# Performance work log

Hardware: AMD Instinct MI355X
Metric: run time of the kernel (lower is better)

## Reference

```python
import jax, jax.numpy as jnp
import numpy as np

N = 100000   # nodes
E = 600000   # edges
IN = 12      # in_dim
H = 128      # hidden_dim
OUT = 2      # out_dim
L = 3        # num_layers
EPS = 1e-5   # BatchNorm eps


def setup_inputs() -> dict:
    key = jax.random.key(0)
    ks = jax.random.split(key, 14)
    s = 0.05
    return {
        "features": jax.random.normal(ks[0], (N, IN), jnp.float32),
        "edge_index": jax.random.randint(ks[1], (2, E), 0, N, dtype=jnp.int32).astype(jnp.int64),
        "emb_W": jax.random.normal(ks[2], (IN, H), jnp.float32) * s,
        "emb_b": jnp.zeros((H,), jnp.float32),
        "Wself": jax.random.normal(ks[3], (L, H, H), jnp.float32) * s,
        "Wneigh": jax.random.normal(ks[4], (L, H, H), jnp.float32) * s,
        "conv_b": jnp.zeros((L, H), jnp.float32),
        "bn_gamma": jnp.ones((L, H), jnp.float32),
        "bn_beta": jnp.zeros((L, H), jnp.float32),
        "W1": jax.random.normal(ks[5], (H, H // 2), jnp.float32) * s,
        "b1": jnp.zeros((H // 2,), jnp.float32),
        "W2": jax.random.normal(ks[6], (H // 2, OUT), jnp.float32) * s,
        "b2": jnp.zeros((OUT,), jnp.float32),
    }


def reference(features, edge_index, emb_W, emb_b, Wself, Wneigh, conv_b,
              bn_gamma, bn_beta, W1, b1, W2, b2):
    src, dst = edge_index[0], edge_index[1]
    # in-degree per destination node (loop-invariant)
    deg = jax.ops.segment_sum(jnp.ones((E,), features.dtype), dst, num_segments=N)
    inv_deg = 1.0 / jnp.maximum(deg, 1.0)  # [N]

    h = features @ emb_W + emb_b           # embedding: [N, H]
    h_last = h
    for i in range(L):
        # SAGEConv 'mean': gather src feats, scatter-sum to dst, divide by degree
        msg_sum = jax.ops.segment_sum(h[src], dst, num_segments=N)  # [N, H]
        h_neigh = msg_sum * inv_deg[:, None]
        h_new = h @ Wself[i] + h_neigh @ Wneigh[i] + conv_b[i]
        # BatchNorm1d over nodes (batch statistics)
        mu = jnp.mean(h_new, axis=0)
        var = jnp.var(h_new, axis=0)
        h_new = (h_new - mu) * jax.lax.rsqrt(var + EPS) * bn_gamma[i] + bn_beta[i]
        h_new = jax.nn.relu(h_new)
        # dropout is identity at inference
        if i > 0:
            h_new = h_new + h_last  # residual
        h_last = h_new
        h = h_new
    # MLP head
    out = jax.nn.relu(h @ W1 + b1) @ W2 + b2  # [N, 2]
    return out
```

## Files before the change

### kernel.cpp

```cpp
#include <hip/hip_runtime.h>
#include <hip/hip_bf16.h>
#include <cstdint>

#define H 128
#define EPS 1e-5f
#define CAP 32

typedef unsigned int uint;
typedef unsigned short ushort;
typedef short short8 __attribute__((ext_vector_type(8)));
typedef float f32x4 __attribute__((ext_vector_type(4)));

__device__ __forceinline__ ushort f2bf(float f) {
  uint u = __float_as_uint(f);
  u += 0x7fffu + ((u >> 16) & 1u);
  return (ushort)(u >> 16);
}
__device__ __forceinline__ float bflo(uint v) { return __uint_as_float(v << 16); }
__device__ __forceinline__ float bfhi(uint v) { return __uint_as_float(v & 0xffff0000u); }

__device__ __forceinline__ int load_idx(const void* ei, long long pos, int is64) {
  if (is64) return (int)((const long long*)ei)[pos];
  return ((const int*)ei)[pos];
}

__global__ __launch_bounds__(256) void k_init(const void* __restrict__ ei, int N,
                                              uint* __restrict__ cnt, int* __restrict__ flag,
                                              const float* __restrict__ F, const float* __restrict__ embW,
                                              const float* __restrict__ embB,
                                              ushort* __restrict__ bufA, ushort* __restrict__ bufB,
                                              const float* __restrict__ Wself, const float* __restrict__ Wneigh,
                                              const float* __restrict__ W1,
                                              ushort* __restrict__ Wsw, ushort* __restrict__ W1sw,
                                              int ZB, int EB) {
  __shared__ float sW[12 * 128];
  __shared__ float sF[256 * 12];
  int b = blockIdx.x, t = threadIdx.x;
  if (b < ZB) {
    int i = b * 256 + t;
    if (i < N) cnt[i] = 0u;
    if (b == 0 && t == 0) {
      const long long* p = (const long long*)ei;
      int ok = 1;
      for (int j = 0; j < 16; ++j) {
        long long s = p[j];
        if (s < 0 || s >= (long long)N) ok = 0;
      }
      *flag = ok;
    }
    return;
  }
  if (b < ZB + EB) {
    int blk = b - ZB;
    for (int i = t; i < 12 * 128; i += 256) sW[i] = embW[i];
    int row0 = blk * 256;
    int nrows = min(256, N - row0);
    for (int i = t; i < nrows * 12; i += 256) sF[i] = F[(size_t)row0 * 12 + i];
    __syncthreads();
    int col = t & 127, half = t >> 7;
    float bias = embB[col];
    int rlo = half * 128, rhi = min(nrows, rlo + 128);
    for (int r = rlo; r < rhi; ++r) {
      float acc = bias;
#pragma unroll
      for (int k = 0; k < 12; ++k) acc = fmaf(sF[r * 12 + k], sW[k * 128 + col], acc);
      bufA[(size_t)(row0 + r) * H + col] = f2bf(acc);
    }
    if (blk == 0 && t < 128) {
      bufA[(size_t)N * H + t] = 0;
      bufB[(size_t)N * H + t] = 0;
    }
    return;
  }
  int e = (b - ZB - EB) * 256 + t;
  if (e < 3 * 4096) {
    int l = e >> 12, r = e & 4095;
    int kt = r >> 9, nt = (r >> 6) & 7, lane = r & 63;
    int quad = lane >> 4, l16 = lane & 15;
    int n = nt * 16 + l16;
    ushort* dst = Wsw + ((size_t)l * 4096 + (kt * 8 + nt) * 64 + lane) * 8;
#pragma unroll
    for (int j = 0; j < 8; ++j) {
      int k = kt * 32 + quad * 8 + j;
      float v = (k < 128) ? Wself[(size_t)l * H * H + (size_t)k * H + n]
                          : Wneigh[(size_t)l * H * H + (size_t)(k - 128) * H + n];
      dst[j] = f2bf(v);
    }
  } else if (e < 3 * 4096 + 1024) {
    int r = e - 3 * 4096;
    int kt = r >> 8, nt = (r >> 6) & 3, lane = r & 63;
    int quad = lane >> 4, l16 = lane & 15;
    int n = nt * 16 + l16;
    ushort* dst = W1sw + ((size_t)((kt * 4 + nt) * 64 + lane)) * 8;
#pragma unroll
    for (int j = 0; j < 8; ++j) {
      int k = kt * 32 + quad * 8 + j;
      dst[j] = f2bf(W1[(size_t)k * 64 + n]);
    }
  }
}

__global__ __launch_bounds__(256) void k_fill(const void* __restrict__ ei, uint* __restrict__ cnt,
                                              uint* __restrict__ csr, int E,
                                              const int* __restrict__ flag) {
  int e0 = (blockIdx.x * 256 + threadIdx.x) * 2;
  if (e0 >= E) return;
  int is64 = *flag;
  int s0, s1 = -1, d0, d1 = -1;
  bool two = (e0 + 1 < E);
  if (is64) {
    const unsigned long long* p = (const unsigned long long*)ei;
    if (two) {
      ulong2 sv = *(const ulong2*)(p + e0);
      ulong2 dv = *(const ulong2*)(p + E + e0);
      s0 = (int)sv.x; s1 = (int)sv.y; d0 = (int)dv.x; d1 = (int)dv.y;
    } else {
      s0 = (int)p[e0]; d0 = (int)p[E + e0];
    }
  } else {
    const int* p = (const int*)ei;
    if (two) {
      int2 sv = *(const int2*)(p + e0);
      int2 dv = *(const int2*)(p + E + e0);
      s0 = sv.x; s1 = sv.y; d0 = dv.x; d1 = dv.y;
    } else {
      s0 = p[e0]; d0 = p[E + e0];
    }
  }
  uint p0 = atomicAdd(&cnt[d0], 1u);
  if (p0 < (uint)CAP) csr[(size_t)d0 * CAP + p0] = (uint)s0;
  if (two) {
    uint p1 = atomicAdd(&cnt[d1], 1u);
    if (p1 < (uint)CAP) csr[(size_t)d1 * CAP + p1] = (uint)s1;
  }
}

__global__ __launch_bounds__(256) void k_gather(const ushort* __restrict__ h, ushort* __restrict__ msg,
                                                const uint* __restrict__ cnt,
                                                const uint* __restrict__ csr,
                                                float* __restrict__ bn_acc, int N) {
  int tid = threadIdx.x;
  if (blockIdx.x == 0) bn_acc[tid] = 0.f;
  int lane = tid & 63, wave = tid >> 6;
  int group = lane >> 4, l16 = lane & 15;
  int n = blockIdx.x * 16 + wave * 4 + group;
  if (n >= N) return;
  uint rawc = cnt[n];
  uint deg = min(rawc, (uint)CAP);
  const uint* row = csr + (size_t)n * CAP;
  const uint4* hu = (const uint4*)h;
  float a0 = 0.f, a1 = 0.f, a2 = 0.f, a3 = 0.f, a4 = 0.f, a5 = 0.f, a6 = 0.f, a7 = 0.f;
  for (uint k = 0; k < deg; k += 8) {
    uint idx[8];
#pragma unroll
    for (int j = 0; j < 8; ++j) idx[j] = (k + j < deg) ? row[k + j] : (uint)N;
    uint4 v[8];
#pragma unroll
    for (int j = 0; j < 8; ++j) v[j] = hu[(size_t)idx[j] * 16 + l16];
#pragma unroll
    for (int j = 0; j < 8; ++j) {
      a0 += bflo(v[j].x); a1 += bfhi(v[j].x);
      a2 += bflo(v[j].y); a3 += bfhi(v[j].y);
      a4 += bflo(v[j].z); a5 += bfhi(v[j].z);
      a6 += bflo(v[j].w); a7 += bfhi(v[j].w);
    }
  }
  float inv = 1.0f / (float)max(rawc, 1u);
  uint4 o;
  o.x = (uint)f2bf(a0 * inv) | ((uint)f2bf(a1 * inv) << 16);
  o.y = (uint)f2bf(a2 * inv) | ((uint)f2bf(a3 * inv) << 16);
  o.z = (uint)f2bf(a4 * inv) | ((uint)f2bf(a5 * inv) << 16);
  o.w = (uint)f2bf(a6 * inv) | ((uint)f2bf(a7 * inv) << 16);
  ((uint4*)msg)[(size_t)n * 16 + l16] = o;
}

__global__ __launch_bounds__(256, 2) void k_gemm(const ushort* __restrict__ hA, ushort* __restrict__ msgz,
                                                 const ushort* __restrict__ Wsw,
                                                 const float* __restrict__ bias,
                                                 float* __restrict__ bn_acc, int N) {
  __shared__ ushort sB[4096 * 8];
  int tid = threadIdx.x;
  int wave = tid >> 6, lane = tid & 63, quad = lane >> 4, l16 = lane & 15;
  {
    const uint4* src = (const uint4*)Wsw;
    uint4* dst = (uint4*)sB;
#pragma unroll
    for (int i = 0; i < 16; ++i) dst[i * 256 + tid] = src[i * 256 + tid];
  }
  __syncthreads();

  int wrow0 = blockIdx.x * 256 + wave * 64;
  f32x4 acc[4][8];
#pragma unroll
  for (int m = 0; m < 4; ++m)
#pragma unroll
    for (int nt = 0; nt < 8; ++nt) acc[m][nt] = (f32x4){0.f, 0.f, 0.f, 0.f};

  short8 zf8 = {0, 0, 0, 0, 0, 0, 0, 0};
#pragma unroll
  for (int kt = 0; kt < 8; ++kt) {
    const ushort* base = (kt < 4) ? hA : msgz;
    int colb = (kt & 3) * 32 + quad * 8;
    short8 a[4];
#pragma unroll
    for (int m = 0; m < 4; ++m) {
      int row = wrow0 + m * 16 + l16;
      a[m] = (row < N) ? *(const short8*)(base + (size_t)row * H + colb) : zf8;
    }
#pragma unroll
    for (int nt = 0; nt < 8; ++nt) {
      short8 bfr = *(const short8*)(sB + ((kt * 8 + nt) * 64 + lane) * 8);
#pragma unroll
      for (int m = 0; m < 4; ++m)
        acc[m][nt] = __builtin_amdgcn_mfma_f32_16x16x32_bf16(a[m], bfr, acc[m][nt], 0, 0, 0);
    }
  }

  float bs[8];
#pragma unroll
  for (int nt = 0; nt < 8; ++nt) bs[nt] = bias[nt * 16 + l16];
  float ps[8], pq[8];
#pragma unroll
  for (int nt = 0; nt < 8; ++nt) { ps[nt] = 0.f; pq[nt] = 0.f; }
#pragma unroll
  for (int m = 0; m < 4; ++m) {
#pragma unroll
    for (int nt = 0; nt < 8; ++nt) {
      int col = nt * 16 + l16;
#pragma unroll
      for (int r = 0; r < 4; ++r) {
        int row = wrow0 + m * 16 + quad * 4 + r;
        if (row < N) {
          float v = acc[m][nt][r] + bs[nt];
          msgz[(size_t)row * H + col] = f2bf(v);
          ps[nt] += v; pq[nt] += v * v;
        }
      }
    }
  }
  __syncthreads();
  float* red = (float*)sB;
  int wq = wave * 4 + quad;
#pragma unroll
  for (int nt = 0; nt < 8; ++nt) {
    red[(wq * 8 + nt) * 17 + l16] = ps[nt];
    red[2176 + (wq * 8 + nt) * 17 + l16] = pq[nt];
  }
  __syncthreads();
  if (tid < 128) {
    int nt = tid >> 4, lc = tid & 15;
    float s = 0.f, q = 0.f;
#pragma unroll
    for (int w2 = 0; w2 < 16; ++w2) {
      s += red[(w2 * 8 + nt) * 17 + lc];
      q += red[2176 + (w2 * 8 + nt) * 17 + lc];
    }
    atomicAdd(&bn_acc[tid], s);
    atomicAdd(&bn_acc[128 + tid], q);
  }
}

__global__ __launch_bounds__(256) void k_norm(uint4* __restrict__ z, const uint4* __restrict__ hprev,
                                              const float* __restrict__ bn_acc,
                                              const float* __restrict__ gamma,
                                              const float* __restrict__ beta,
                                              int residual, int n4, float invN) {
  __shared__ float ssc[128], ssh[128];
  int t = threadIdx.x;
  if (t < 128) {
    float mu = bn_acc[t] * invN;
    float var = fmaxf(bn_acc[128 + t] * invN - mu * mu, 0.f);
    float sc = gamma[t] * rsqrtf(var + EPS);
    ssc[t] = sc;
    ssh[t] = beta[t] - mu * sc;
  }
  __syncthreads();
  int idx = blockIdx.x * 256 + t;
  if (idx >= n4) return;
  int j = (idx & 15) * 8;
  uint4 v = z[idx];
  float x0 = fmaxf(fmaf(bflo(v.x), ssc[j + 0], ssh[j + 0]), 0.f);
  float x1 = fmaxf(fmaf(bfhi(v.x), ssc[j + 1], ssh[j + 1]), 0.f);
  float x2 = fmaxf(fmaf(bflo(v.y), ssc[j + 2], ssh[j + 2]), 0.f);
  float x3 = fmaxf(fmaf(bfhi(v.y), ssc[j + 3], ssh[j + 3]), 0.f);
  float x4 = fmaxf(fmaf(bflo(v.z), ssc[j + 4], ssh[j + 4]), 0.f);
  float x5 = fmaxf(fmaf(bfhi(v.z), ssc[j + 5], ssh[j + 5]), 0.f);
  float x6 = fmaxf(fmaf(bflo(v.w), ssc[j + 6], ssh[j + 6]), 0.f);
  float x7 = fmaxf(fmaf(bfhi(v.w), ssc[j + 7], ssh[j + 7]), 0.f);
  if (residual) {
    uint4 r = hprev[idx];
    x0 += bflo(r.x); x1 += bfhi(r.x); x2 += bflo(r.y); x3 += bfhi(r.y);
    x4 += bflo(r.z); x5 += bfhi(r.z); x6 += bflo(r.w); x7 += bfhi(r.w);
  }
  uint4 o;
  o.x = (uint)f2bf(x0) | ((uint)f2bf(x1) << 16);
  o.y = (uint)f2bf(x2) | ((uint)f2bf(x3) << 16);
  o.z = (uint)f2bf(x4) | ((uint)f2bf(x5) << 16);
  o.w = (uint)f2bf(x6) | ((uint)f2bf(x7) << 16);
  z[idx] = o;
}

__global__ __launch_bounds__(256) void k_head(const ushort* __restrict__ z, const ushort* __restrict__ hprev,
                                              const float* __restrict__ bn_acc,
                                              const float* __restrict__ gamma,
                                              const float* __restrict__ beta, float invN,
                                              const ushort* __restrict__ W1sw,
                                              const float* __restrict__ b1, const float* __restrict__ W2,
                                              const float* __restrict__ b2, float* __restrict__ out, int N) {
  __shared__ float ssc[128], ssh[128];
  int tid = threadIdx.x;
  if (tid < 128) {
    float mu = bn_acc[tid] * invN;
    float var = fmaxf(bn_acc[128 + tid] * invN - mu * mu, 0.f);
    float sc = gamma[tid] * rsqrtf(var + EPS);
    ssc[tid] = sc;
    ssh[tid] = beta[tid] - mu * sc;
  }
  __syncthreads();
  int wave = tid >> 6, lane = tid & 63, quad = lane >> 4, l16 = lane & 15;
  int wrow0 = blockIdx.x * 64 + wave * 16;
  int am = wrow0 + l16;
  bool avalid = am < N;
  short8 af[4];
#pragma unroll
  for (int kt = 0; kt < 4; ++kt) {
    int c0 = kt * 32 + quad * 8;
    uint4 vz = avalid ? ((const uint4*)z)[(size_t)am * 16 + kt * 4 + quad] : make_uint4(0, 0, 0, 0);
    uint4 vr = avalid ? ((const uint4*)hprev)[(size_t)am * 16 + kt * 4 + quad] : make_uint4(0, 0, 0, 0);
    float x0 = fmaxf(fmaf(bflo(vz.x), ssc[c0 + 0], ssh[c0 + 0]), 0.f) + bflo(vr.x);
    float x1 = fmaxf(fmaf(bfhi(vz.x), ssc[c0 + 1], ssh[c0 + 1]), 0.f) + bfhi(vr.x);
    float x2 = fmaxf(fmaf(bflo(vz.y), ssc[c0 + 2], ssh[c0 + 2]), 0.f) + bflo(vr.y);
    float x3 = fmaxf(fmaf(bfhi(vz.y), ssc[c0 + 3], ssh[c0 + 3]), 0.f) + bfhi(vr.y);
    float x4 = fmaxf(fmaf(bflo(vz.z), ssc[c0 + 4], ssh[c0 + 4]), 0.f) + bflo(vr.z);
    float x5 = fmaxf(fmaf(bfhi(vz.z), ssc[c0 + 5], ssh[c0 + 5]), 0.f) + bfhi(vr.z);
    float x6 = fmaxf(fmaf(bflo(vz.w), ssc[c0 + 6], ssh[c0 + 6]), 0.f) + bflo(vr.w);
    float x7 = fmaxf(fmaf(bfhi(vz.w), ssc[c0 + 7], ssh[c0 + 7]), 0.f) + bfhi(vr.w);
    ushort u[8] = {f2bf(x0), f2bf(x1), f2bf(x2), f2bf(x3), f2bf(x4), f2bf(x5), f2bf(x6), f2bf(x7)};
    af[kt] = *(short8*)u;
  }
  const short8* Bp = (const short8*)W1sw;
  f32x4 acc[4];
#pragma unroll
  for (int nt = 0; nt < 4; ++nt) acc[nt] = (f32x4){0.f, 0.f, 0.f, 0.f};
#pragma unroll
  for (int kt = 0; kt < 4; ++kt) {
#pragma unroll
    for (int nt = 0; nt < 4; ++nt) {
      short8 bfr = Bp[(kt * 4 + nt) * 64 + lane];
      acc[nt] = __builtin_amdgcn_mfma_f32_16x16x32_bf16(af[kt], bfr, acc[nt], 0, 0, 0);
    }
  }
  float p0[4] = {0.f, 0.f, 0.f, 0.f}, p1[4] = {0.f, 0.f, 0.f, 0.f};
#pragma unroll
  for (int nt = 0; nt < 4; ++nt) {
    int c = nt * 16 + l16;
    float bc = b1[c], w20 = W2[c * 2], w21 = W2[c * 2 + 1];
#pragma unroll
    for (int r = 0; r < 4; ++r) {
      float v = fmaxf(acc[nt][r] + bc, 0.f);
      p0[r] = fmaf(v, w20, p0[r]);
      p1[r] = fmaf(v, w21, p1[r]);
    }
  }
#pragma unroll
  for (int m = 1; m < 16; m <<= 1) {
#pragma unroll
    for (int r = 0; r < 4; ++r) {
      p0[r] += __shfl_xor(p0[r], m);
      p1[r] += __shfl_xor(p1[r], m);
    }
  }
  if (l16 == 0) {
    float b20 = b2[0], b21 = b2[1];
#pragma unroll
    for (int r = 0; r < 4; ++r) {
      int row = wrow0 + quad * 4 + r;
      if (row < N) {
        float2 o = make_float2(p0[r] + b20, p1[r] + b21);
        *(float2*)(out + (size_t)row * 2) = o;
      }
    }
  }
}

extern "C" void kernel_launch(void* const* d_in, const int* in_sizes, int n_in,
                              void* d_out, int out_size, void* d_ws, size_t ws_size,
                              hipStream_t stream) {
  const float* features = (const float*)d_in[0];
  const void*  edges    = d_in[1];
  const float* emb_W    = (const float*)d_in[2];
  const float* emb_b    = (const float*)d_in[3];
  const float* Wself    = (const float*)d_in[4];
  const float* Wneigh   = (const float*)d_in[5];
  const float* conv_b   = (const float*)d_in[6];
  const float* bn_gamma = (const float*)d_in[7];
  const float* bn_beta  = (const float*)d_in[8];
  const float* W1       = (const float*)d_in[9];
  const float* b1       = (const float*)d_in[10];
  const float* W2       = (const float*)d_in[11];
  const float* b2       = (const float*)d_in[12];
  float* out = (float*)d_out;
  const int N = in_sizes[0] / 12;
  const int E = in_sizes[1] / 2;
  const float invN = 1.0f / (float)N;

  char* ws = (char*)d_ws;
  size_t off = 0;
  auto take = [&](size_t bytes) {
    char* p = ws + off;
    off = (off + bytes + 511) & ~(size_t)511;
    return p;
  };
  int*    flag   = (int*)take(4);
  uint*   cnt    = (uint*)take((size_t)N * 4);
  uint*   csr    = (uint*)take((size_t)N * CAP * 4);
  float*  bn_acc = (float*)take(256 * 4);
  ushort* Wsw    = (ushort*)take(3 * 4096 * 8 * 2);
  ushort* W1sw   = (ushort*)take(1024 * 8 * 2);
  ushort* bufA   = (ushort*)take(((size_t)N + 1) * H * 2);
  ushort* bufB   = (ushort*)take(((size_t)N + 1) * H * 2);

  const int ZB = (N + 255) / 256;
  const int EB = (N + 255) / 256;
  const int PB = (3 * 4096 + 1024 + 255) / 256;
  const int FB = (E + 511) / 512;
  const int GB = (N + 255) / 256;

  k_init<<<ZB + EB + PB, 256, 0, stream>>>(edges, N, cnt, flag, features, emb_W, emb_b,
                                           bufA, bufB, Wself, Wneigh, W1, Wsw, W1sw, ZB, EB);
  k_fill<<<FB, 256, 0, stream>>>(edges, cnt, csr, E, flag);

  ushort* hbuf = bufA;
  ushort* obuf = bufB;
  const int n4 = N * 16;
  for (int i = 0; i < 3; ++i) {
    k_gather<<<(N + 15) / 16, 256, 0, stream>>>(hbuf, obuf, cnt, csr, bn_acc, N);
    k_gemm<<<GB, 256, 0, stream>>>(hbuf, obuf, Wsw + (size_t)i * 4096 * 8,
                                   conv_b + (size_t)i * H, bn_acc, N);
    if (i < 2) {
      k_norm<<<(n4 + 255) / 256, 256, 0, stream>>>((uint4*)obuf, (const uint4*)hbuf, bn_acc,
                                                   bn_gamma + (size_t)i * H, bn_beta + (size_t)i * H,
                                                   (i > 0) ? 1 : 0, n4, invN);
      ushort* t = hbuf; hbuf = obuf; obuf = t;
    }
  }
  k_head<<<(N + 63) / 64, 256, 0, stream>>>(obuf, hbuf, bn_acc, bn_gamma + 2 * H, bn_beta + 2 * H,
                                            invN, W1sw, b1, W2, b2, out, N);
}
```

Measured before the change: 348.9 us.

## Halve GEMM tile and LDS, stage weights in two halves, bank BN atomics

The GEMM kernel now covers 128 rows per block instead of 256 and keeps only half the weight matrix in LDS at a time. The second half is held in registers and swapped into LDS between the self and neighbor K-phases. This cuts LDS and accumulator register use so up to 4 blocks can share a CU, and it doubles the grid size. BatchNorm statistic atomics are also spread over 16 banks to reduce contention, at the cost of extra barriers, more weight reloads per row, and a small bank-summing loop in the norm and head kernels.

After: 357.5 us. +2.4%, slower.

```diff
diff --git a/kernel.cpp b/kernel.cpp
--- a/kernel.cpp
+++ b/kernel.cpp
@@ -5,6 +5,7 @@
 #define H 128
 #define EPS 1e-5f
 #define CAP 32
+#define NB 16
 
 typedef unsigned int uint;
 typedef unsigned short ushort;
@@ -140,7 +141,10 @@
                                                 const uint* __restrict__ csr,
                                                 float* __restrict__ bn_acc, int N) {
   int tid = threadIdx.x;
-  if (blockIdx.x == 0) bn_acc[tid] = 0.f;
+  if (blockIdx.x == 0) {
+#pragma unroll
+    for (int i = tid; i < NB * 256; i += 256) bn_acc[i] = 0.f;
+  }
   int lane = tid & 63, wave = tid >> 6;
   int group = lane >> 4, l16 = lane & 15;
   int n = blockIdx.x * 16 + wave * 4 + group;
@@ -174,44 +178,69 @@
   ((uint4*)msg)[(size_t)n * 16 + l16] = o;
 }
 
-__global__ __launch_bounds__(256, 2) void k_gemm(const ushort* __restrict__ hA, ushort* __restrict__ msgz,
+__global__ __launch_bounds__(256, 4) void k_gemm(const ushort* __restrict__ hA, ushort* __restrict__ msgz,
                                                  const ushort* __restrict__ Wsw,
                                                  const float* __restrict__ bias,
                                                  float* __restrict__ bn_acc, int N) {
-  __shared__ ushort sB[4096 * 8];
+  __shared__ ushort sB[2048 * 8];
   int tid = threadIdx.x;
   int wave = tid >> 6, lane = tid & 63, quad = lane >> 4, l16 = lane & 15;
+  const uint4* wsrc = (const uint4*)Wsw;
+  uint4* dst = (uint4*)sB;
+  uint4 w2[8];
   {
-    const uint4* src = (const uint4*)Wsw;
-    uint4* dst = (uint4*)sB;
-#pragma unroll
-    for (int i = 0; i < 16; ++i) dst[i * 256 + tid] = src[i * 256 + tid];
-  }
-  __syncthreads();
-
-  int wrow0 = blockIdx.x * 256 + wave * 64;
-  f32x4 acc[4][8];
-#pragma unroll
-  for (int m = 0; m < 4; ++m)
+#pragma unroll
+    for (int i = 0; i < 8; ++i) dst[i * 256 + tid] = wsrc[i * 256 + tid];
+#pragma unroll
+    for (int i = 0; i < 8; ++i) w2[i] = wsrc[2048 + i * 256 + tid];
+  }
+  __syncthreads();
+
+  int wrow0 = blockIdx.x * 128 + wave * 32;
+  f32x4 acc[2][8];
+#pragma unroll
+  for (int m = 0; m < 2; ++m)
 #pragma unroll
     for (int nt = 0; nt < 8; ++nt) acc[m][nt] = (f32x4){0.f, 0.f, 0.f, 0.f};
 
   short8 zf8 = {0, 0, 0, 0, 0, 0, 0, 0};
 #pragma unroll
-  for (int kt = 0; kt < 8; ++kt) {
-    const ushort* base = (kt < 4) ? hA : msgz;
-    int colb = (kt & 3) * 32 + quad * 8;
-    short8 a[4];
-#pragma unroll
-    for (int m = 0; m < 4; ++m) {
+  for (int kt = 0; kt < 4; ++kt) {
+    int colb = kt * 32 + quad * 8;
+    short8 a[2];
+#pragma unroll
+    for (int m = 0; m < 2; ++m) {
       int row = wrow0 + m * 16 + l16;
-      a[m] = (row < N) ? *(const short8*)(base + (size_t)row * H + colb) : zf8;
+      a[m] = (row < N) ? *(const short8*)(hA + (size_t)row * H + colb) : zf8;
     }
 #pragma unroll
     for (int nt = 0; nt < 8; ++nt) {
       short8 bfr = *(const short8*)(sB + ((kt * 8 + nt) * 64 + lane) * 8);
 #pragma unroll
-      for (int m = 0; m < 4; ++m)
+      for (int m = 0; m < 2; ++m)
+        acc[m][nt] = __builtin_amdgcn_mfma_f32_16x16x32_bf16(a[m], bfr, acc[m][nt], 0, 0, 0);
+    }
+  }
+  __syncthreads();
+  {
+#pragma unroll
+    for (int i = 0; i < 8; ++i) dst[i * 256 + tid] = w2[i];
+  }
+  __syncthreads();
+#pragma unroll
+  for (int kt = 0; kt < 4; ++kt) {
+    int colb = kt * 32 + quad * 8;
+    short8 a[2];
+#pragma unroll
+    for (int m = 0; m < 2; ++m) {
+      int row = wrow0 + m * 16 + l16;
+      a[m] = (row < N) ? *(const short8*)(msgz + (size_t)row * H + colb) : zf8;
+    }
+#pragma unroll
+    for (int nt = 0; nt < 8; ++nt) {
+      short8 bfr = *(const short8*)(sB + ((kt * 8 + nt) * 64 + lane) * 8);
+#pragma unroll
+      for (int m = 0; m < 2; ++m)
         acc[m][nt] = __builtin_amdgcn_mfma_f32_16x16x32_bf16(a[m], bfr, acc[m][nt], 0, 0, 0);
     }
   }
@@ -223,7 +252,7 @@
 #pragma unroll
   for (int nt = 0; nt < 8; ++nt) { ps[nt] = 0.f; pq[nt] = 0.f; }
 #pragma unroll
-  for (int m = 0; m < 4; ++m) {
+  for (int m = 0; m < 2; ++m) {
 #pragma unroll
     for (int nt = 0; nt < 8; ++nt) {
       int col = nt * 16 + l16;
@@ -251,12 +280,13 @@
     int nt = tid >> 4, lc = tid & 15;
     float s = 0.f, q = 0.f;
 #pragma unroll
-    for (int w2 = 0; w2 < 16; ++w2) {
-      s += red[(w2 * 8 + nt) * 17 + lc];
-      q += red[2176 + (w2 * 8 + nt) * 17 + lc];
-    }
-    atomicAdd(&bn_acc[tid], s);
-    atomicAdd(&bn_acc[128 + tid], q);
+    for (int w2i = 0; w2i < 16; ++w2i) {
+      s += red[(w2i * 8 + nt) * 17 + lc];
+      q += red[2176 + (w2i * 8 + nt) * 17 + lc];
+    }
+    float* bank = bn_acc + (size_t)(blockIdx.x & (NB - 1)) * 256;
+    atomicAdd(&bank[tid], s);
+    atomicAdd(&bank[128 + tid], q);
   }
 }
 
@@ -268,8 +298,14 @@
   __shared__ float ssc[128], ssh[128];
   int t = threadIdx.x;
   if (t < 128) {
-    float mu = bn_acc[t] * invN;
-    float var = fmaxf(bn_acc[128 + t] * invN - mu * mu, 0.f);
+    float s = 0.f, q = 0.f;
+#pragma unroll
+    for (int b = 0; b < NB; ++b) {
+      s += bn_acc[b * 256 + t];
+      q += bn_acc[b * 256 + 128 + t];
+    }
+    float mu = s * invN;
+    float var = fmaxf(q * invN - mu * mu, 0.f);
     float sc = gamma[t] * rsqrtf(var + EPS);
     ssc[t] = sc;
     ssh[t] = beta[t] - mu * sc;
@@ -310,8 +346,14 @@
   __shared__ float ssc[128], ssh[128];
   int tid = threadIdx.x;
   if (tid < 128) {
-    float mu = bn_acc[tid] * invN;
-    float var = fmaxf(bn_acc[128 + tid] * invN - mu * mu, 0.f);
+    float s = 0.f, q = 0.f;
+#pragma unroll
+    for (int b = 0; b < NB; ++b) {
+      s += bn_acc[b * 256 + tid];
+      q += bn_acc[b * 256 + 128 + tid];
+    }
+    float mu = s * invN;
+    float var = fmaxf(q * invN - mu * mu, 0.f);
     float sc = gamma[tid] * rsqrtf(var + EPS);
     ssc[tid] = sc;
     ssh[tid] = beta[tid] - mu * sc;
@@ -414,7 +456,7 @@
   int*    flag   = (int*)take(4);
   uint*   cnt    = (uint*)take((size_t)N * 4);
   uint*   csr    = (uint*)take((size_t)N * CAP * 4);
-  float*  bn_acc = (float*)take(256 * 4);
+  float*  bn_acc = (float*)take(NB * 256 * 4);
   ushort* Wsw    = (ushort*)take(3 * 4096 * 8 * 2);
   ushort* W1sw   = (ushort*)take(1024 * 8 * 2);
   ushort* bufA   = (ushort*)take(((size_t)N + 1) * H * 2);
@@ -424,7 +466,7 @@
   const int EB = (N + 255) / 256;
   const int PB = (3 * 4096 + 1024 + 255) / 256;
   const int FB = (E + 511) / 512;
-  const int GB = (N + 255) / 256;
+  const int GB = (N + 127) / 128;
 
   k_init<<<ZB + EB + PB, 256, 0, stream>>>(edges, N, cnt, flag, features, emb_W, emb_b,
                                            bufA, bufB, Wself, Wneigh, W1, Wsw, W1sw, ZB, EB);
```
